# Kernel tuning notes

Hardware: AMD Instinct MI355X
Metric: run time of the kernel (lower is better)

The kernel has to match this reference:

```python
import jax, jax.numpy as jnp
import numpy as np

B, T, M, P, N2 = 16, 8192, 128, 128, 128  # N2 = N//2 complex modes

def setup_inputs() -> dict:
    key = jax.random.key(0)
    k1, k2, k3, k4, k5 = jax.random.split(key, 5)
    u = jax.random.normal(k1, (B, T, M), dtype=jnp.float32)
    # log-parametrized Lambda (S5 'log' convention): Lambda = -exp(row0) + 1j*row1
    log_re = jnp.log(jax.random.uniform(k2, (N2,), minval=0.1, maxval=1.0))
    im = jnp.pi * jnp.arange(N2, dtype=jnp.float32)  # HiPPO-like imaginary spread
    Lambda_param = jnp.stack([log_re, im], axis=0).astype(jnp.float32)
    B_param = jax.random.normal(k3, (2, N2, M), dtype=jnp.float32) / np.sqrt(M)
    C_param = jax.random.normal(k4, (2, P, N2), dtype=jnp.float32) / np.sqrt(N2)
    delta = jnp.array([0.01], dtype=jnp.float32)  # default_\u0394
    return {"u": u, "Lambda_param": Lambda_param, "B_param": B_param,
            "C_param": C_param, "delta": delta}

def reference(u, Lambda_param, B_param, C_param, delta):
    # Reconstruct complex continuous-time matrices
    Lam = (-jnp.exp(Lambda_param[0]) + 1j * Lambda_param[1]).astype(jnp.complex64)   # (N2,)
    Bc = (B_param[0] + 1j * B_param[1]).astype(jnp.complex64)                        # (N2, M)
    Cc = (C_param[0] + 1j * C_param[1]).astype(jnp.complex64)                        # (P, N2)
    d = delta[0]
    # ZOH discretization: Lambda_d = exp(Lam*d), Bd = ((Lambda_d - 1)/Lam) * B
    Ld = jnp.exp(Lam * d)                                                            # (N2,)
    Bd = ((Ld - 1.0) / Lam)[:, None] * Bc                                            # (N2, M)
    # Input projection: Bu[b,t,n] = sum_m u[b,t,m] * Bd[n,m]
    Bu = jnp.einsum('btm,nm->btn', u.astype(jnp.complex64), Bd)                      # (B,T,N2)
    # Parallel scan of x_{k+1} = Ld * x_k + Bu_k, x_0 = 0 -> x holds x_1..x_T
    A = jnp.broadcast_to(Ld, Bu.shape)
    def comb(e1, e2):
        a1, b1 = e1
        a2, b2 = e2
        return (a1 * a2, a2 * b1 + b2)
    _, x = jax.lax.associative_scan(comb, (A, Bu), axis=1)                           # (B,T,N2)
    # return_next_y=True: y_k = 2*Re(C x_{k+1})
    y = 2.0 * jnp.real(jnp.einsum('btn,pn->btp', x, Cc))                             # (B,T,P)
    return y
```

## Files before the change

kernel.cpp:

```cpp
#include <hip/hip_runtime.h>
#include <hip/hip_bf16.h>

#define LCH 128
#define NCH 64
#define NCHUNKS 1024

typedef __attribute__((ext_vector_type(8))) short short8v;
typedef __attribute__((ext_vector_type(4))) short short4v;
typedef __attribute__((ext_vector_type(4))) float f32x4;

#define W2_LDINV 0
#define W2_LDP   16384
#define W2_E     32768
#define W2_CIN   163840
#define WS_WPACK_BYTE  (589824 * 4)
#define WS_CCPACK_BYTE (589824 * 4 + 65536)

#define BUS_BYTE(s, np) ((((s) >> 3) * 4096) + ((np) * 16) + (((s) & 7) * 2))

__device__ inline unsigned short f2bf(float f) {
    union { __hip_bfloat16 h; unsigned short u; } v;
    v.h = __float2bfloat16(f);
    return v.u;
}
__device__ inline short4v pack4(float a, float b, float c, float d) {
    union { __hip_bfloat162 h2[2]; short4v s4; } pk;
    pk.h2[0] = __float22bfloat162_rn(make_float2(a, b));
    pk.h2[1] = __float22bfloat162_rn(make_float2(c, d));
    return pk.s4;
}

__global__ void k0_pows(const float* __restrict__ lp, const float* __restrict__ delta,
                        float2* __restrict__ ws2) {
    const int r = blockIdx.x;
    const int tid = threadIdx.x;
    const int n = tid & 127;
    const double d = (double)delta[0];
    const double lre = -exp((double)lp[n]);
    const double lim = (double)lp[128 + n];
    const double kk = (double)(r + 1) * d;
    if (tid < 128) {
        const double mag = exp(-lre * kk);
        ws2[W2_LDINV + r * 128 + n] = make_float2((float)(mag * cos(lim * kk)),
                                                  (float)(-mag * sin(lim * kk)));
    } else {
        const double mag = exp(lre * kk);
        ws2[W2_LDP + r * 128 + n] = make_float2((float)(mag * cos(lim * kk)),
                                                (float)(mag * sin(lim * kk)));
    }
}

__global__ void k0_wpack(const float* __restrict__ lp, const float* __restrict__ bp,
                         const float* __restrict__ delta, unsigned short* __restrict__ wpack) {
    const int gid = blockIdx.x * 512 + threadIdx.x;
    const int j = gid & 7;
    const int lane = (gid >> 3) & 63;
    const int ks = (gid >> 9) & 3;
    const int ntile = gid >> 11;
    const int np = ntile * 16 + (lane & 15);
    const int m = ks * 32 + ((lane >> 4) & 3) * 8 + j;
    const int n = np & 127;
    const double d = (double)delta[0];
    const double lre = -exp((double)lp[n]);
    const double lim = (double)lp[128 + n];
    const double er = exp(lre * d);
    const double ldr = er * cos(lim * d), ldi = er * sin(lim * d);
    const double nr = ldr - 1.0, ni = ldi;
    const double den = lre * lre + lim * lim;
    const double cr = (nr * lre + ni * lim) / den;
    const double ci = (ni * lre - nr * lim) / den;
    const double br = (double)bp[n * 128 + m];
    const double bi = (double)bp[16384 + n * 128 + m];
    const double v = (np < 128) ? (cr * br - ci * bi) : (cr * bi + ci * br);
    wpack[gid] = f2bf((float)v);
}

__global__ void k0_cpack(const float* __restrict__ cp, unsigned short* __restrict__ ccpack) {
    const int gid = blockIdx.x * 512 + threadIdx.x;
    const int j = gid & 7;
    const int lane = (gid >> 3) & 63;
    const int ks = (gid >> 9) & 7;
    const int ptile = gid >> 12;
    const int p = ptile * 16 + (lane & 15);
    const int k = ks * 32 + ((lane >> 4) & 3) * 8 + j;
    const int n = k >> 1;
    const float v = ((k & 1) == 0) ? 2.0f * cp[p * 128 + n] : -2.0f * cp[16384 + p * 128 + n];
    ccpack[gid] = f2bf(v);
}

__device__ inline void stage_u(const float* __restrict__ uchunk, unsigned short* lds_u) {
    const float4* uf = (const float4*)uchunk;
    const int tid = threadIdx.x;
#pragma unroll
    for (int it = 0; it < 8; ++it) {
        const int f4 = it * 512 + tid;
        const float4 v = uf[f4];
        const int t = f4 >> 5;
        const int m = (f4 & 31) * 4;
        const int byte = (t * 256 + m * 2) ^ ((t & 7) << 4);
        *(short4v*)((char*)lds_u + byte) = pack4(v.x, v.y, v.z, v.w);
    }
}

__global__ __launch_bounds__(512, 4) void k1_end(const float* __restrict__ u,
                                                 float2* __restrict__ ws2,
                                                 const unsigned short* __restrict__ wpack) {
    __shared__ unsigned short lds_u[16384];
    const int tid = threadIdx.x;
    const int lane = tid & 63;
    const int w = tid >> 6;
    const int tl = lane & 15;
    const int gq = (lane >> 4) & 3;
    const int g = blockIdx.x;
    const int b = g >> 6;
    const int c = g & 63;
    const int n = w * 16 + tl;
    stage_u(u + (size_t)(b * 8192 + c * 128) * 128, lds_u);
    __syncthreads();
    const short8v* wp = (const short8v*)wpack;
    float er = 0.f, ei = 0.f;
#pragma unroll
    for (int h = 0; h < 2; ++h) {
        f32x4 acc[4][2];
#pragma unroll
        for (int i = 0; i < 4; ++i) { acc[i][0] = (f32x4)0.f; acc[i][1] = (f32x4)0.f; }
        __builtin_amdgcn_s_setprio(1);
#pragma unroll
        for (int ks = 0; ks < 4; ++ks) {
            const short8v b0 = wp[(w * 4 + ks) * 64 + lane];
            const short8v b1 = wp[((8 + w) * 4 + ks) * 64 + lane];
#pragma unroll
            for (int tt2 = 0; tt2 < 4; ++tt2) {
                const int t = (h * 4 + tt2) * 16 + tl;
                const int byte = (t * 256 + (ks * 32 + gq * 8) * 2) ^ ((t & 7) << 4);
                const short8v a = *(const short8v*)((const char*)lds_u + byte);
                acc[tt2][0] = __builtin_amdgcn_mfma_f32_16x16x32_bf16(a, b0, acc[tt2][0], 0, 0, 0);
                acc[tt2][1] = __builtin_amdgcn_mfma_f32_16x16x32_bf16(a, b1, acc[tt2][1], 0, 0, 0);
            }
        }
        __builtin_amdgcn_s_setprio(0);
        __builtin_amdgcn_sched_barrier(0);
#pragma unroll
        for (int tt2 = 0; tt2 < 4; ++tt2) {
#pragma unroll
            for (int reg = 0; reg < 4; ++reg) {
                const int r = (h * 4 + tt2) * 16 + gq * 4 + reg;
                const float2 li = ws2[W2_LDINV + r * 128 + n];
                const float br = acc[tt2][0][reg], bi = acc[tt2][1][reg];
                er += li.x * br - li.y * bi;
                ei += li.x * bi + li.y * br;
            }
        }
        __builtin_amdgcn_sched_barrier(0);
    }
    er += __shfl_xor(er, 16); ei += __shfl_xor(ei, 16);
    er += __shfl_xor(er, 32); ei += __shfl_xor(ei, 32);
    const float2 ld = ws2[W2_LDP + 127 * 128 + n];
    if (lane < 16) {
        ws2[W2_E + g * 128 + n] = make_float2(ld.x * er - ld.y * ei,
                                              ld.x * ei + ld.y * er);
    }
}

__global__ void k2_carry(float2* __restrict__ ws2) {
    const int idx = blockIdx.x * 256 + threadIdx.x;
    const int b = idx >> 7;
    const int n = idx & 127;
    const float2 l = ws2[W2_LDP + 127 * 128 + n];
    float cr = 0.f, ci = 0.f;
    for (int c = 0; c < NCH; ++c) {
        const int o = (b * NCH + c) * 128 + n;
        ws2[W2_CIN + o] = make_float2(cr, ci);
        const float2 e = ws2[W2_E + o];
        const float nr = fmaf(l.x, cr, fmaf(-l.y, ci, e.x));
        const float ni = fmaf(l.x, ci, fmaf(l.y, cr, e.y));
        cr = nr; ci = ni;
    }
}

__global__ __launch_bounds__(512, 4) void k3_main(const float* __restrict__ u,
                                                  const float2* __restrict__ ws2,
                                                  const unsigned short* __restrict__ wpack,
                                                  const unsigned short* __restrict__ ccpack,
                                                  float* __restrict__ y) {
    __shared__ unsigned short lds[32768];
    unsigned short* lds_u = lds;
    const int tid = threadIdx.x;
    const int lane = tid & 63;
    const int w = tid >> 6;
    const int tl = lane & 15;
    const int gq = (lane >> 4) & 3;
    const int g = blockIdx.x;
    const int b = g >> 6;
    const int c = g & 63;
    const int n = w * 16 + tl;

    stage_u(u + (size_t)(b * 8192 + c * 128) * 128, lds_u);
    __syncthreads();

    const short8v* wp = (const short8v*)wpack;
#pragma unroll
    for (int hh = 0; hh < 2; ++hh) {
        const int h = 1 - hh;
        f32x4 acc[4][2];
#pragma unroll
        for (int i = 0; i < 4; ++i) { acc[i][0] = (f32x4)0.f; acc[i][1] = (f32x4)0.f; }
        __builtin_amdgcn_s_setprio(1);
#pragma unroll
        for (int ks = 0; ks < 4; ++ks) {
            const short8v b0 = wp[(w * 4 + ks) * 64 + lane];
            const short8v b1 = wp[((8 + w) * 4 + ks) * 64 + lane];
#pragma unroll
            for (int tt2 = 0; tt2 < 4; ++tt2) {
                const int t = (h * 4 + tt2) * 16 + tl;
                const int byte = (t * 256 + (ks * 32 + gq * 8) * 2) ^ ((t & 7) << 4);
                const short8v a = *(const short8v*)((const char*)lds_u + byte);
                acc[tt2][0] = __builtin_amdgcn_mfma_f32_16x16x32_bf16(a, b0, acc[tt2][0], 0, 0, 0);
                acc[tt2][1] = __builtin_amdgcn_mfma_f32_16x16x32_bf16(a, b1, acc[tt2][1], 0, 0, 0);
            }
        }
        __builtin_amdgcn_s_setprio(0);
        __builtin_amdgcn_sched_barrier(0);
        if (h == 0) __syncthreads();
#pragma unroll
        for (int tt2 = 0; tt2 < 4; ++tt2) {
            float vr[4], vi[4];
#pragma unroll
            for (int reg = 0; reg < 4; ++reg) {
                const int r = (h * 4 + tt2) * 16 + gq * 4 + reg;
                const float2 li = ws2[W2_LDINV + r * 128 + n];
                const float br = acc[tt2][0][reg], bi = acc[tt2][1][reg];
                vr[reg] = li.x * br - li.y * bi;
                vi[reg] = li.x * bi + li.y * br;
            }
            const int s0 = (h * 4 + tt2) * 16 + gq * 4;
            const int rowr = w * 16 + tl;
            const int rowi = 128 + rowr;
            *(short4v*)((char*)lds + BUS_BYTE(s0, rowr)) = pack4(vr[0], vr[1], vr[2], vr[3]);
            *(short4v*)((char*)lds + BUS_BYTE(s0, rowi)) = pack4(vi[0], vi[1], vi[2], vi[3]);
        }
        __builtin_amdgcn_sched_barrier(0);
    }

    short8v ONES, D0, D1;
#pragma unroll
    for (int j = 0; j < 8; ++j) {
        const int sl = gq * 8 + j;
        ONES[j] = (short)0x3F80;
        D0[j] = (sl <= tl) ? (short)0x3F80 : (short)0;
        D1[j] = (sl <= tl + 16) ? (short)0x3F80 : (short)0;
    }
    f32x4 z[8][2];
#pragma unroll
    for (int i = 0; i < 8; ++i) { z[i][0] = (f32x4)0.f; z[i][1] = (f32x4)0.f; }
#pragma unroll
    for (int ks = 0; ks < 4; ++ks) {
        const int sb = ks * 32 + gq * 8;
        const int rowr = w * 16 + tl;
        const int rowi = 128 + rowr;
        const short8v b0 = *(const short8v*)((const char*)lds + BUS_BYTE(sb, rowr));
        const short8v b1 = *(const short8v*)((const char*)lds + BUS_BYTE(sb, rowi));
#pragma unroll
        for (int tt = 0; tt < 8; ++tt) {
            if (tt < 2 * ks) continue;
            const short8v a = (tt == 2 * ks) ? D0 : ((tt == 2 * ks + 1) ? D1 : ONES);
            z[tt][0] = __builtin_amdgcn_mfma_f32_16x16x32_bf16(a, b0, z[tt][0], 0, 0, 0);
            z[tt][1] = __builtin_amdgcn_mfma_f32_16x16x32_bf16(a, b1, z[tt][1], 0, 0, 0);
        }
    }
    __syncthreads();

    const float2 cin = ws2[W2_CIN + g * 128 + n];
#pragma unroll
    for (int tt = 0; tt < 8; ++tt) {
#pragma unroll
        for (int reg = 0; reg < 4; ++reg) {
            const int r = tt * 16 + gq * 4 + reg;
            const float2 ld = ws2[W2_LDP + r * 128 + n];
            const float zr = z[tt][0][reg] + cin.x;
            const float zi = z[tt][1][reg] + cin.y;
            const float xr = ld.x * zr - ld.y * zi;
            const float xi = ld.x * zi + ld.y * zr;
            union { __hip_bfloat162 h2; unsigned uu; } pk;
            pk.h2 = __float22bfloat162_rn(make_float2(xr, xi));
            const int byte = (r * 512 + n * 4) ^ ((r & 7) << 4);
            *(unsigned*)((char*)lds + byte) = pk.uu;
        }
    }
    __syncthreads();

    const short8v* cc = (const short8v*)ccpack;
    f32x4 yac[8];
#pragma unroll
    for (int i = 0; i < 8; ++i) yac[i] = (f32x4)0.f;
    __builtin_amdgcn_s_setprio(1);
#pragma unroll
    for (int ks = 0; ks < 8; ++ks) {
        const short8v bfrg = cc[(w * 8 + ks) * 64 + lane];
#pragma unroll
        for (int tt = 0; tt < 8; ++tt) {
            const int t = tt * 16 + tl;
            const int byte = (t * 512 + (ks * 32 + gq * 8) * 2) ^ ((t & 7) << 4);
            const short8v a = *(const short8v*)((const char*)lds + byte);
            yac[tt] = __builtin_amdgcn_mfma_f32_16x16x32_bf16(a, bfrg, yac[tt], 0, 0, 0);
        }
    }
    __builtin_amdgcn_s_setprio(0);
    const int p = w * 16 + tl;
    float* yrow = y + (size_t)(b * 8192 + c * 128) * 128;
#pragma unroll
    for (int tt = 0; tt < 8; ++tt) {
#pragma unroll
        for (int reg = 0; reg < 4; ++reg) {
            const int t = tt * 16 + gq * 4 + reg;
            yrow[t * 128 + p] = yac[tt][reg];
        }
    }
}

extern "C" void kernel_launch(void* const* d_in, const int* in_sizes, int n_in,
                              void* d_out, int out_size, void* d_ws, size_t ws_size,
                              hipStream_t stream) {
    const float* u     = (const float*)d_in[0];
    const float* lp    = (const float*)d_in[1];
    const float* bp    = (const float*)d_in[2];
    const float* cp    = (const float*)d_in[3];
    const float* delta = (const float*)d_in[4];
    float* y  = (float*)d_out;
    float2* ws2 = (float2*)d_ws;
    unsigned short* wpack  = (unsigned short*)((char*)d_ws + WS_WPACK_BYTE);
    unsigned short* ccpack = (unsigned short*)((char*)d_ws + WS_CCPACK_BYTE);

    k0_pows <<<128, 256, 0, stream>>>(lp, delta, ws2);
    k0_wpack<<<64, 512, 0, stream>>>(lp, bp, delta, wpack);
    k0_cpack<<<64, 512, 0, stream>>>(cp, ccpack);
    k1_end  <<<NCHUNKS, 512, 0, stream>>>(u, ws2, wpack);
    k2_carry<<<8, 256, 0, stream>>>(ws2);
    k3_main <<<NCHUNKS, 512, 0, stream>>>(u, ws2, wpack, ccpack, y);
}
```

Measured before the change: 88.36 us.

## Process two chunks per block and prefetch next chunk's input into registers

k1_end and k3_main now handle CPB=2 consecutive chunks per workgroup, so half as many blocks are launched. The next chunk's u tile is loaded into registers while the current chunk is being computed, hiding global load latency behind the MFMA work. The cost is extra register pressure from holding the prefetched float4 values and more barriers per block. With 512 blocks on a GPU with many CUs, occupancy and parallelism drop.

```diff
diff --git a/kernel.cpp b/kernel.cpp
--- a/kernel.cpp
+++ b/kernel.cpp
@@ -4,6 +4,7 @@
 #define LCH 128
 #define NCH 64
 #define NCHUNKS 1024
+#define CPB 2
 
 typedef __attribute__((ext_vector_type(8))) short short8v;
 typedef __attribute__((ext_vector_type(4))) short short4v;
@@ -88,17 +89,15 @@
     ccpack[gid] = f2bf(v);
 }
 
-__device__ inline void stage_u(const float* __restrict__ uchunk, unsigned short* lds_u) {
-    const float4* uf = (const float4*)uchunk;
+__device__ inline void stage_regs(const float4* pre, unsigned short* lds_u) {
     const int tid = threadIdx.x;
 #pragma unroll
     for (int it = 0; it < 8; ++it) {
         const int f4 = it * 512 + tid;
-        const float4 v = uf[f4];
         const int t = f4 >> 5;
         const int m = (f4 & 31) * 4;
         const int byte = (t * 256 + m * 2) ^ ((t & 7) << 4);
-        *(short4v*)((char*)lds_u + byte) = pack4(v.x, v.y, v.z, v.w);
+        *(short4v*)((char*)lds_u + byte) = pack4(pre[it].x, pre[it].y, pre[it].z, pre[it].w);
     }
 }
 
@@ -111,54 +110,73 @@
     const int w = tid >> 6;
     const int tl = lane & 15;
     const int gq = (lane >> 4) & 3;
-    const int g = blockIdx.x;
-    const int b = g >> 6;
-    const int c = g & 63;
+    const int g0 = blockIdx.x * CPB;
+    const int b = g0 >> 6;
+    const int c0 = g0 & 63;
     const int n = w * 16 + tl;
-    stage_u(u + (size_t)(b * 8192 + c * 128) * 128, lds_u);
-    __syncthreads();
     const short8v* wp = (const short8v*)wpack;
-    float er = 0.f, ei = 0.f;
-#pragma unroll
-    for (int h = 0; h < 2; ++h) {
-        f32x4 acc[4][2];
-#pragma unroll
-        for (int i = 0; i < 4; ++i) { acc[i][0] = (f32x4)0.f; acc[i][1] = (f32x4)0.f; }
-        __builtin_amdgcn_s_setprio(1);
-#pragma unroll
-        for (int ks = 0; ks < 4; ++ks) {
-            const short8v b0 = wp[(w * 4 + ks) * 64 + lane];
-            const short8v b1 = wp[((8 + w) * 4 + ks) * 64 + lane];
+
+    float4 pre[8];
+    {
+        const float4* uf = (const float4*)(u + (size_t)(b * 8192 + c0 * 128) * 128);
+#pragma unroll
+        for (int it = 0; it < 8; ++it) pre[it] = uf[it * 512 + tid];
+    }
+
+#pragma unroll
+    for (int cc = 0; cc < CPB; ++cc) {
+        const int g = g0 + cc;
+        __syncthreads();
+        stage_regs(pre, lds_u);
+        __syncthreads();
+        if (cc + 1 < CPB) {
+            const float4* uf1 = (const float4*)(u + (size_t)(b * 8192 + (c0 + cc + 1) * 128) * 128);
+#pragma unroll
+            for (int it = 0; it < 8; ++it) pre[it] = uf1[it * 512 + tid];
+            __builtin_amdgcn_sched_barrier(0);
+        }
+        float er = 0.f, ei = 0.f;
+#pragma unroll
+        for (int h = 0; h < 2; ++h) {
+            f32x4 acc[4][2];
+#pragma unroll
+            for (int i = 0; i < 4; ++i) { acc[i][0] = (f32x4)0.f; acc[i][1] = (f32x4)0.f; }
+            __builtin_amdgcn_s_setprio(1);
+#pragma unroll
+            for (int ks = 0; ks < 4; ++ks) {
+                const short8v b0 = wp[(w * 4 + ks) * 64 + lane];
+                const short8v b1 = wp[((8 + w) * 4 + ks) * 64 + lane];
+#pragma unroll
+                for (int tt2 = 0; tt2 < 4; ++tt2) {
+                    const int t = (h * 4 + tt2) * 16 + tl;
+                    const int byte = (t * 256 + (ks * 32 + gq * 8) * 2) ^ ((t & 7) << 4);
+                    const short8v a = *(const short8v*)((const char*)lds_u + byte);
+                    acc[tt2][0] = __builtin_amdgcn_mfma_f32_16x16x32_bf16(a, b0, acc[tt2][0], 0, 0, 0);
+                    acc[tt2][1] = __builtin_amdgcn_mfma_f32_16x16x32_bf16(a, b1, acc[tt2][1], 0, 0, 0);
+                }
+            }
+            __builtin_amdgcn_s_setprio(0);
+            __builtin_amdgcn_sched_barrier(0);
 #pragma unroll
             for (int tt2 = 0; tt2 < 4; ++tt2) {
-                const int t = (h * 4 + tt2) * 16 + tl;
-                const int byte = (t * 256 + (ks * 32 + gq * 8) * 2) ^ ((t & 7) << 4);
-                const short8v a = *(const short8v*)((const char*)lds_u + byte);
-                acc[tt2][0] = __builtin_amdgcn_mfma_f32_16x16x32_bf16(a, b0, acc[tt2][0], 0, 0, 0);
-                acc[tt2][1] = __builtin_amdgcn_mfma_f32_16x16x32_bf16(a, b1, acc[tt2][1], 0, 0, 0);
-            }
-        }
-        __builtin_amdgcn_s_setprio(0);
-        __builtin_amdgcn_sched_barrier(0);
-#pragma unroll
-        for (int tt2 = 0; tt2 < 4; ++tt2) {
-#pragma unroll
-            for (int reg = 0; reg < 4; ++reg) {
-                const int r = (h * 4 + tt2) * 16 + gq * 4 + reg;
-                const float2 li = ws2[W2_LDINV + r * 128 + n];
-                const float br = acc[tt2][0][reg], bi = acc[tt2][1][reg];
-                er += li.x * br - li.y * bi;
-                ei += li.x * bi + li.y * br;
-            }
-        }
-        __builtin_amdgcn_sched_barrier(0);
-    }
-    er += __shfl_xor(er, 16); ei += __shfl_xor(ei, 16);
-    er += __shfl_xor(er, 32); ei += __shfl_xor(ei, 32);
-    const float2 ld = ws2[W2_LDP + 127 * 128 + n];
-    if (lane < 16) {
-        ws2[W2_E + g * 128 + n] = make_float2(ld.x * er - ld.y * ei,
-                                              ld.x * ei + ld.y * er);
+#pragma unroll
+                for (int reg = 0; reg < 4; ++reg) {
+                    const int r = (h * 4 + tt2) * 16 + gq * 4 + reg;
+                    const float2 li = ws2[W2_LDINV + r * 128 + n];
+                    const float br = acc[tt2][0][reg], bi = acc[tt2][1][reg];
+                    er += li.x * br - li.y * bi;
+                    ei += li.x * bi + li.y * br;
+                }
+            }
+            __builtin_amdgcn_sched_barrier(0);
+        }
+        er += __shfl_xor(er, 16); ei += __shfl_xor(ei, 16);
+        er += __shfl_xor(er, 32); ei += __shfl_xor(ei, 32);
+        const float2 ld = ws2[W2_LDP + 127 * 128 + n];
+        if (lane < 16) {
+            ws2[W2_E + g * 128 + n] = make_float2(ld.x * er - ld.y * ei,
+                                                  ld.x * ei + ld.y * er);
+        }
     }
 }
 
@@ -184,136 +202,155 @@
                                                   const unsigned short* __restrict__ ccpack,
                                                   float* __restrict__ y) {
     __shared__ unsigned short lds[32768];
-    unsigned short* lds_u = lds;
     const int tid = threadIdx.x;
     const int lane = tid & 63;
     const int w = tid >> 6;
     const int tl = lane & 15;
     const int gq = (lane >> 4) & 3;
-    const int g = blockIdx.x;
-    const int b = g >> 6;
-    const int c = g & 63;
+    const int g0 = blockIdx.x * CPB;
+    const int b = g0 >> 6;
+    const int c0 = g0 & 63;
     const int n = w * 16 + tl;
-
-    stage_u(u + (size_t)(b * 8192 + c * 128) * 128, lds_u);
-    __syncthreads();
-
     const short8v* wp = (const short8v*)wpack;
-#pragma unroll
-    for (int hh = 0; hh < 2; ++hh) {
-        const int h = 1 - hh;
-        f32x4 acc[4][2];
-#pragma unroll
-        for (int i = 0; i < 4; ++i) { acc[i][0] = (f32x4)0.f; acc[i][1] = (f32x4)0.f; }
-        __builtin_amdgcn_s_setprio(1);
+    const short8v* cc8 = (const short8v*)ccpack;
+
+    float4 pre[8];
+    {
+        const float4* uf = (const float4*)(u + (size_t)(b * 8192 + c0 * 128) * 128);
+#pragma unroll
+        for (int it = 0; it < 8; ++it) pre[it] = uf[it * 512 + tid];
+    }
+
+#pragma unroll
+    for (int cc = 0; cc < CPB; ++cc) {
+        const int g = g0 + cc;
+        const int c = c0 + cc;
+        __syncthreads();
+        stage_regs(pre, lds);
+        __syncthreads();
+
+#pragma unroll
+        for (int hh = 0; hh < 2; ++hh) {
+            const int h = 1 - hh;
+            f32x4 acc[4][2];
+#pragma unroll
+            for (int i = 0; i < 4; ++i) { acc[i][0] = (f32x4)0.f; acc[i][1] = (f32x4)0.f; }
+            __builtin_amdgcn_s_setprio(1);
+#pragma unroll
+            for (int ks = 0; ks < 4; ++ks) {
+                const short8v b0 = wp[(w * 4 + ks) * 64 + lane];
+                const short8v b1 = wp[((8 + w) * 4 + ks) * 64 + lane];
+#pragma unroll
+                for (int tt2 = 0; tt2 < 4; ++tt2) {
+                    const int t = (h * 4 + tt2) * 16 + tl;
+                    const int byte = (t * 256 + (ks * 32 + gq * 8) * 2) ^ ((t & 7) << 4);
+                    const short8v a = *(const short8v*)((const char*)lds + byte);
+                    acc[tt2][0] = __builtin_amdgcn_mfma_f32_16x16x32_bf16(a, b0, acc[tt2][0], 0, 0, 0);
+                    acc[tt2][1] = __builtin_amdgcn_mfma_f32_16x16x32_bf16(a, b1, acc[tt2][1], 0, 0, 0);
+                }
+            }
+            __builtin_amdgcn_s_setprio(0);
+            __builtin_amdgcn_sched_barrier(0);
+            if (h == 0) __syncthreads();
+#pragma unroll
+            for (int tt2 = 0; tt2 < 4; ++tt2) {
+                float vr[4], vi[4];
+#pragma unroll
+                for (int reg = 0; reg < 4; ++reg) {
+                    const int r = (h * 4 + tt2) * 16 + gq * 4 + reg;
+                    const float2 li = ws2[W2_LDINV + r * 128 + n];
+                    const float br = acc[tt2][0][reg], bi = acc[tt2][1][reg];
+                    vr[reg] = li.x * br - li.y * bi;
+                    vi[reg] = li.x * bi + li.y * br;
+                }
+                const int s0 = (h * 4 + tt2) * 16 + gq * 4;
+                const int rowr = w * 16 + tl;
+                const int rowi = 128 + rowr;
+                *(short4v*)((char*)lds + BUS_BYTE(s0, rowr)) = pack4(vr[0], vr[1], vr[2], vr[3]);
+                *(short4v*)((char*)lds + BUS_BYTE(s0, rowi)) = pack4(vi[0], vi[1], vi[2], vi[3]);
+            }
+            __builtin_amdgcn_sched_barrier(0);
+        }
+
+        if (cc + 1 < CPB) {
+            const float4* uf1 = (const float4*)(u + (size_t)(b * 8192 + (c + 1) * 128) * 128);
+#pragma unroll
+            for (int it = 0; it < 8; ++it) pre[it] = uf1[it * 512 + tid];
+            __builtin_amdgcn_sched_barrier(0);
+        }
+
+        short8v ONES, D0, D1;
+#pragma unroll
+        for (int j = 0; j < 8; ++j) {
+            const int sl = gq * 8 + j;
+            ONES[j] = (short)0x3F80;
+            D0[j] = (sl <= tl) ? (short)0x3F80 : (short)0;
+            D1[j] = (sl <= tl + 16) ? (short)0x3F80 : (short)0;
+        }
+        f32x4 z[8][2];
+#pragma unroll
+        for (int i = 0; i < 8; ++i) { z[i][0] = (f32x4)0.f; z[i][1] = (f32x4)0.f; }
 #pragma unroll
         for (int ks = 0; ks < 4; ++ks) {
-            const short8v b0 = wp[(w * 4 + ks) * 64 + lane];
-            const short8v b1 = wp[((8 + w) * 4 + ks) * 64 + lane];
-#pragma unroll
-            for (int tt2 = 0; tt2 < 4; ++tt2) {
-                const int t = (h * 4 + tt2) * 16 + tl;
-                const int byte = (t * 256 + (ks * 32 + gq * 8) * 2) ^ ((t & 7) << 4);
-                const short8v a = *(const short8v*)((const char*)lds_u + byte);
-                acc[tt2][0] = __builtin_amdgcn_mfma_f32_16x16x32_bf16(a, b0, acc[tt2][0], 0, 0, 0);
-                acc[tt2][1] = __builtin_amdgcn_mfma_f32_16x16x32_bf16(a, b1, acc[tt2][1], 0, 0, 0);
-            }
-        }
-        __builtin_amdgcn_s_setprio(0);
-        __builtin_amdgcn_sched_barrier(0);
-        if (h == 0) __syncthreads();
-#pragma unroll
-        for (int tt2 = 0; tt2 < 4; ++tt2) {
-            float vr[4], vi[4];
-#pragma unroll
-            for (int reg = 0; reg < 4; ++reg) {
-                const int r = (h * 4 + tt2) * 16 + gq * 4 + reg;
-                const float2 li = ws2[W2_LDINV + r * 128 + n];
-                const float br = acc[tt2][0][reg], bi = acc[tt2][1][reg];
-                vr[reg] = li.x * br - li.y * bi;
-                vi[reg] = li.x * bi + li.y * br;
-            }
-            const int s0 = (h * 4 + tt2) * 16 + gq * 4;
+            const int sb = ks * 32 + gq * 8;
             const int rowr = w * 16 + tl;
             const int rowi = 128 + rowr;
-            *(short4v*)((char*)lds + BUS_BYTE(s0, rowr)) = pack4(vr[0], vr[1], vr[2], vr[3]);
-            *(short4v*)((char*)lds + BUS_BYTE(s0, rowi)) = pack4(vi[0], vi[1], vi[2], vi[3]);
-        }
-        __builtin_amdgcn_sched_barrier(0);
-    }
-
-    short8v ONES, D0, D1;
-#pragma unroll
-    for (int j = 0; j < 8; ++j) {
-        const int sl = gq * 8 + j;
-        ONES[j] = (short)0x3F80;
-        D0[j] = (sl <= tl) ? (short)0x3F80 : (short)0;
-        D1[j] = (sl <= tl + 16) ? (short)0x3F80 : (short)0;
-    }
-    f32x4 z[8][2];
-#pragma unroll
-    for (int i = 0; i < 8; ++i) { z[i][0] = (f32x4)0.f; z[i][1] = (f32x4)0.f; }
-#pragma unroll
-    for (int ks = 0; ks < 4; ++ks) {
-        const int sb = ks * 32 + gq * 8;
-        const int rowr = w * 16 + tl;
-        const int rowi = 128 + rowr;
-        const short8v b0 = *(const short8v*)((const char*)lds + BUS_BYTE(sb, rowr));
-        const short8v b1 = *(const short8v*)((const char*)lds + BUS_BYTE(sb, rowi));
+            const short8v b0 = *(const short8v*)((const char*)lds + BUS_BYTE(sb, rowr));
+            const short8v b1 = *(const short8v*)((const char*)lds + BUS_BYTE(sb, rowi));
+#pragma unroll
+            for (int tt = 0; tt < 8; ++tt) {
+                if (tt < 2 * ks) continue;
+                const short8v a = (tt == 2 * ks) ? D0 : ((tt == 2 * ks + 1) ? D1 : ONES);
+                z[tt][0] = __builtin_amdgcn_mfma_f32_16x16x32_bf16(a, b0, z[tt][0], 0, 0, 0);
+                z[tt][1] = __builtin_amdgcn_mfma_f32_16x16x32_bf16(a, b1, z[tt][1], 0, 0, 0);
+            }
+        }
+        __syncthreads();
+
+        const float2 cin = ws2[W2_CIN + g * 128 + n];
 #pragma unroll
         for (int tt = 0; tt < 8; ++tt) {
-            if (tt < 2 * ks) continue;
-            const short8v a = (tt == 2 * ks) ? D0 : ((tt == 2 * ks + 1) ? D1 : ONES);
-            z[tt][0] = __builtin_amdgcn_mfma_f32_16x16x32_bf16(a, b0, z[tt][0], 0, 0, 0);
-            z[tt][1] = __builtin_amdgcn_mfma_f32_16x16x32_bf16(a, b1, z[tt][1], 0, 0, 0);
-        }
-    }
-    __syncthreads();
-
-    const float2 cin = ws2[W2_CIN + g * 128 + n];
-#pragma unroll
-    for (int tt = 0; tt < 8; ++tt) {
-#pragma unroll
-        for (int reg = 0; reg < 4; ++reg) {
-            const int r = tt * 16 + gq * 4 + reg;
-            const float2 ld = ws2[W2_LDP + r * 128 + n];
-            const float zr = z[tt][0][reg] + cin.x;
-            const float zi = z[tt][1][reg] + cin.y;
-            const float xr = ld.x * zr - ld.y * zi;
-            const float xi = ld.x * zi + ld.y * zr;
-            union { __hip_bfloat162 h2; unsigned uu; } pk;
-            pk.h2 = __float22bfloat162_rn(make_float2(xr, xi));
-            const int byte = (r * 512 + n * 4) ^ ((r & 7) << 4);
-            *(unsigned*)((char*)lds + byte) = pk.uu;
-        }
-    }
-    __syncthreads();
-
-    const short8v* cc = (const short8v*)ccpack;
-    f32x4 yac[8];
-#pragma unroll
-    for (int i = 0; i < 8; ++i) yac[i] = (f32x4)0.f;
-    __builtin_amdgcn_s_setprio(1);
-#pragma unroll
-    for (int ks = 0; ks < 8; ++ks) {
-        const short8v bfrg = cc[(w * 8 + ks) * 64 + lane];
+#pragma unroll
+            for (int reg = 0; reg < 4; ++reg) {
+                const int r = tt * 16 + gq * 4 + reg;
+                const float2 ld = ws2[W2_LDP + r * 128 + n];
+                const float zr = z[tt][0][reg] + cin.x;
+                const float zi = z[tt][1][reg] + cin.y;
+                const float xr = ld.x * zr - ld.y * zi;
+                const float xi = ld.x * zi + ld.y * zr;
+                union { __hip_bfloat162 h2; unsigned uu; } pk;
+                pk.h2 = __float22bfloat162_rn(make_float2(xr, xi));
+                const int byte = (r * 512 + n * 4) ^ ((r & 7) << 4);
+                *(unsigned*)((char*)lds + byte) = pk.uu;
+            }
+        }
+        __syncthreads();
+
+        f32x4 yac[8];
+#pragma unroll
+        for (int i = 0; i < 8; ++i) yac[i] = (f32x4)0.f;
+        __builtin_amdgcn_s_setprio(1);
+#pragma unroll
+        for (int ks = 0; ks < 8; ++ks) {
+            const short8v bfrg = cc8[(w * 8 + ks) * 64 + lane];
+#pragma unroll
+            for (int tt = 0; tt < 8; ++tt) {
+                const int t = tt * 16 + tl;
+                const int byte = (t * 512 + (ks * 32 + gq * 8) * 2) ^ ((t & 7) << 4);
+                const short8v a = *(const short8v*)((const char*)lds + byte);
+                yac[tt] = __builtin_amdgcn_mfma_f32_16x16x32_bf16(a, bfrg, yac[tt], 0, 0, 0);
+            }
+        }
+        __builtin_amdgcn_s_setprio(0);
+        const int p = w * 16 + tl;
+        float* yrow = y + (size_t)(b * 8192 + c * 128) * 128;
 #pragma unroll
         for (int tt = 0; tt < 8; ++tt) {
-            const int t = tt * 16 + tl;
-            const int byte = (t * 512 + (ks * 32 + gq * 8) * 2) ^ ((t & 7) << 4);
-            const short8v a = *(const short8v*)((const char*)lds + byte);
-            yac[tt] = __builtin_amdgcn_mfma_f32_16x16x32_bf16(a, bfrg, yac[tt], 0, 0, 0);
-        }
-    }
-    __builtin_amdgcn_s_setprio(0);
-    const int p = w * 16 + tl;
-    float* yrow = y + (size_t)(b * 8192 + c * 128) * 128;
-#pragma unroll
-    for (int tt = 0; tt < 8; ++tt) {
-#pragma unroll
-        for (int reg = 0; reg < 4; ++reg) {
-            const int t = tt * 16 + gq * 4 + reg;
-            yrow[t * 128 + p] = yac[tt][reg];
+#pragma unroll
+            for (int reg = 0; reg < 4; ++reg) {
+                const int t = tt * 16 + gq * 4 + reg;
+                yrow[t * 128 + p] = yac[tt][reg];
+            }
         }
     }
 }
@@ -334,7 +371,7 @@
     k0_pows <<<128, 256, 0, stream>>>(lp, delta, ws2);
     k0_wpack<<<64, 512, 0, stream>>>(lp, bp, delta, wpack);
     k0_cpack<<<64, 512, 0, stream>>>(cp, ccpack);
-    k1_end  <<<NCHUNKS, 512, 0, stream>>>(u, ws2, wpack);
+    k1_end  <<<NCHUNKS / CPB, 512, 0, stream>>>(u, ws2, wpack);
     k2_carry<<<8, 256, 0, stream>>>(ws2);
-    k3_main <<<NCHUNKS, 512, 0, stream>>>(u, ws2, wpack, ccpack, y);
-}
+    k3_main <<<NCHUNKS / CPB, 512, 0, stream>>>(u, ws2, wpack, ccpack, y);
+}
```

Measured after the change: 320.2 us. +262.4%, slower.

## Halve scan chunk length to 64, fuse setup kernels, reuse carry buffer in place

Applied to the files above, without the earlier changes.

Chunk length drops from 128 to 64 timesteps, so the grid grows to 2048 blocks with half the LDS each, and launch bounds rise to 6 blocks per CU for more occupancy. The intra-chunk triangular scan does less work per chunk, but the sequential carry pass now walks 128 chunks per batch instead of 64. The three setup kernels are merged into one launch to cut launch overhead, and the carry kernel writes carries over the chunk-end buffer in place instead of using a separate array.

```diff
diff --git a/kernel.cpp b/kernel.cpp
--- a/kernel.cpp
+++ b/kernel.cpp
@@ -1,20 +1,19 @@
 #include <hip/hip_runtime.h>
 #include <hip/hip_bf16.h>
 
-#define LCH 128
-#define NCH 64
-#define NCHUNKS 1024
+#define LCH 64
+#define NCH 128
+#define NCHUNKS 2048
 
 typedef __attribute__((ext_vector_type(8))) short short8v;
 typedef __attribute__((ext_vector_type(4))) short short4v;
 typedef __attribute__((ext_vector_type(4))) float f32x4;
 
 #define W2_LDINV 0
-#define W2_LDP   16384
-#define W2_E     32768
-#define W2_CIN   163840
-#define WS_WPACK_BYTE  (589824 * 4)
-#define WS_CCPACK_BYTE (589824 * 4 + 65536)
+#define W2_LDP   8192
+#define W2_E     16384
+#define WS_WPACK_BYTE  2359296
+#define WS_CCPACK_BYTE (2359296 + 65536)
 
 #define BUS_BYTE(s, np) ((((s) >> 3) * 4096) + ((np) * 16) + (((s) & 7) * 2))
 
@@ -30,132 +29,129 @@
     return pk.s4;
 }
 
-__global__ void k0_pows(const float* __restrict__ lp, const float* __restrict__ delta,
-                        float2* __restrict__ ws2) {
+__global__ void k0_all(const float* __restrict__ lp, const float* __restrict__ bp,
+                       const float* __restrict__ cp, const float* __restrict__ delta,
+                       float2* __restrict__ ws2, unsigned short* __restrict__ wpack,
+                       unsigned short* __restrict__ ccpack) {
     const int r = blockIdx.x;
     const int tid = threadIdx.x;
-    const int n = tid & 127;
-    const double d = (double)delta[0];
-    const double lre = -exp((double)lp[n]);
-    const double lim = (double)lp[128 + n];
-    const double kk = (double)(r + 1) * d;
-    if (tid < 128) {
-        const double mag = exp(-lre * kk);
-        ws2[W2_LDINV + r * 128 + n] = make_float2((float)(mag * cos(lim * kk)),
-                                                  (float)(-mag * sin(lim * kk)));
+    if (r < 64) {
+        if (tid < 256) {
+            const int n = tid & 127;
+            const double d = (double)delta[0];
+            const double lre = -exp((double)lp[n]);
+            const double lim = (double)lp[128 + n];
+            const double kk = (double)(r + 1) * d;
+            if (tid < 128) {
+                const double mag = exp(-lre * kk);
+                ws2[W2_LDINV + r * 128 + n] = make_float2((float)(mag * cos(lim * kk)),
+                                                          (float)(-mag * sin(lim * kk)));
+            } else {
+                const double mag = exp(lre * kk);
+                ws2[W2_LDP + r * 128 + n] = make_float2((float)(mag * cos(lim * kk)),
+                                                        (float)(mag * sin(lim * kk)));
+            }
+        }
+    } else if (r < 128) {
+        const int gid = (r - 64) * 512 + tid;
+        const int j = gid & 7;
+        const int lane = (gid >> 3) & 63;
+        const int ks = (gid >> 9) & 3;
+        const int ntile = gid >> 11;
+        const int np = ntile * 16 + (lane & 15);
+        const int m = ks * 32 + ((lane >> 4) & 3) * 8 + j;
+        const int n = np & 127;
+        const double d = (double)delta[0];
+        const double lre = -exp((double)lp[n]);
+        const double lim = (double)lp[128 + n];
+        const double er = exp(lre * d);
+        const double ldr = er * cos(lim * d), ldi = er * sin(lim * d);
+        const double nr = ldr - 1.0, ni = ldi;
+        const double den = lre * lre + lim * lim;
+        const double cr = (nr * lre + ni * lim) / den;
+        const double ci = (ni * lre - nr * lim) / den;
+        const double br = (double)bp[n * 128 + m];
+        const double bi = (double)bp[16384 + n * 128 + m];
+        const double v = (np < 128) ? (cr * br - ci * bi) : (cr * bi + ci * br);
+        wpack[gid] = f2bf((float)v);
     } else {
-        const double mag = exp(lre * kk);
-        ws2[W2_LDP + r * 128 + n] = make_float2((float)(mag * cos(lim * kk)),
-                                                (float)(mag * sin(lim * kk)));
-    }
-}
-
-__global__ void k0_wpack(const float* __restrict__ lp, const float* __restrict__ bp,
-                         const float* __restrict__ delta, unsigned short* __restrict__ wpack) {
-    const int gid = blockIdx.x * 512 + threadIdx.x;
-    const int j = gid & 7;
-    const int lane = (gid >> 3) & 63;
-    const int ks = (gid >> 9) & 3;
-    const int ntile = gid >> 11;
-    const int np = ntile * 16 + (lane & 15);
-    const int m = ks * 32 + ((lane >> 4) & 3) * 8 + j;
-    const int n = np & 127;
-    const double d = (double)delta[0];
-    const double lre = -exp((double)lp[n]);
-    const double lim = (double)lp[128 + n];
-    const double er = exp(lre * d);
-    const double ldr = er * cos(lim * d), ldi = er * sin(lim * d);
-    const double nr = ldr - 1.0, ni = ldi;
-    const double den = lre * lre + lim * lim;
-    const double cr = (nr * lre + ni * lim) / den;
-    const double ci = (ni * lre - nr * lim) / den;
-    const double br = (double)bp[n * 128 + m];
-    const double bi = (double)bp[16384 + n * 128 + m];
-    const double v = (np < 128) ? (cr * br - ci * bi) : (cr * bi + ci * br);
-    wpack[gid] = f2bf((float)v);
-}
-
-__global__ void k0_cpack(const float* __restrict__ cp, unsigned short* __restrict__ ccpack) {
-    const int gid = blockIdx.x * 512 + threadIdx.x;
-    const int j = gid & 7;
-    const int lane = (gid >> 3) & 63;
-    const int ks = (gid >> 9) & 7;
-    const int ptile = gid >> 12;
-    const int p = ptile * 16 + (lane & 15);
-    const int k = ks * 32 + ((lane >> 4) & 3) * 8 + j;
-    const int n = k >> 1;
-    const float v = ((k & 1) == 0) ? 2.0f * cp[p * 128 + n] : -2.0f * cp[16384 + p * 128 + n];
-    ccpack[gid] = f2bf(v);
-}
-
-__device__ inline void stage_u(const float* __restrict__ uchunk, unsigned short* lds_u) {
-    const float4* uf = (const float4*)uchunk;
-    const int tid = threadIdx.x;
-#pragma unroll
-    for (int it = 0; it < 8; ++it) {
-        const int f4 = it * 512 + tid;
-        const float4 v = uf[f4];
-        const int t = f4 >> 5;
-        const int m = (f4 & 31) * 4;
-        const int byte = (t * 256 + m * 2) ^ ((t & 7) << 4);
-        *(short4v*)((char*)lds_u + byte) = pack4(v.x, v.y, v.z, v.w);
-    }
-}
-
-__global__ __launch_bounds__(512, 4) void k1_end(const float* __restrict__ u,
+        const int gid = (r - 128) * 512 + tid;
+        const int j = gid & 7;
+        const int lane = (gid >> 3) & 63;
+        const int ks = (gid >> 9) & 7;
+        const int ptile = gid >> 12;
+        const int p = ptile * 16 + (lane & 15);
+        const int k = ks * 32 + ((lane >> 4) & 3) * 8 + j;
+        const int n = k >> 1;
+        const float v = ((k & 1) == 0) ? 2.0f * cp[p * 128 + n]
+                                       : -2.0f * cp[16384 + p * 128 + n];
+        ccpack[gid] = f2bf(v);
+    }
+}
+
+__global__ __launch_bounds__(512, 6) void k1_end(const float* __restrict__ u,
                                                  float2* __restrict__ ws2,
                                                  const unsigned short* __restrict__ wpack) {
-    __shared__ unsigned short lds_u[16384];
+    __shared__ unsigned short lds_u[8192];
     const int tid = threadIdx.x;
     const int lane = tid & 63;
     const int w = tid >> 6;
     const int tl = lane & 15;
     const int gq = (lane >> 4) & 3;
     const int g = blockIdx.x;
-    const int b = g >> 6;
-    const int c = g & 63;
+    const int b = g >> 7;
+    const int c = g & 127;
     const int n = w * 16 + tl;
-    stage_u(u + (size_t)(b * 8192 + c * 128) * 128, lds_u);
-    __syncthreads();
     const short8v* wp = (const short8v*)wpack;
+
+    {
+        const float4* uf = (const float4*)(u + (size_t)(b * 8192 + c * LCH) * 128);
+#pragma unroll
+        for (int it = 0; it < 4; ++it) {
+            const int f4 = it * 512 + tid;
+            const float4 v = uf[f4];
+            const int t = f4 >> 5;
+            const int m = (f4 & 31) * 4;
+            const int byte = (t * 256 + m * 2) ^ ((t & 7) << 4);
+            *(short4v*)((char*)lds_u + byte) = pack4(v.x, v.y, v.z, v.w);
+        }
+    }
+    __syncthreads();
+
+    f32x4 acc[4][2];
+#pragma unroll
+    for (int i = 0; i < 4; ++i) { acc[i][0] = (f32x4)0.f; acc[i][1] = (f32x4)0.f; }
+    __builtin_amdgcn_s_setprio(1);
+#pragma unroll
+    for (int ks = 0; ks < 4; ++ks) {
+        const short8v b0 = wp[(w * 4 + ks) * 64 + lane];
+        const short8v b1 = wp[((8 + w) * 4 + ks) * 64 + lane];
+#pragma unroll
+        for (int tt = 0; tt < 4; ++tt) {
+            const int t = tt * 16 + tl;
+            const int byte = (t * 256 + (ks * 32 + gq * 8) * 2) ^ ((t & 7) << 4);
+            const short8v a = *(const short8v*)((const char*)lds_u + byte);
+            acc[tt][0] = __builtin_amdgcn_mfma_f32_16x16x32_bf16(a, b0, acc[tt][0], 0, 0, 0);
+            acc[tt][1] = __builtin_amdgcn_mfma_f32_16x16x32_bf16(a, b1, acc[tt][1], 0, 0, 0);
+        }
+    }
+    __builtin_amdgcn_s_setprio(0);
+
     float er = 0.f, ei = 0.f;
 #pragma unroll
-    for (int h = 0; h < 2; ++h) {
-        f32x4 acc[4][2];
-#pragma unroll
-        for (int i = 0; i < 4; ++i) { acc[i][0] = (f32x4)0.f; acc[i][1] = (f32x4)0.f; }
-        __builtin_amdgcn_s_setprio(1);
-#pragma unroll
-        for (int ks = 0; ks < 4; ++ks) {
-            const short8v b0 = wp[(w * 4 + ks) * 64 + lane];
-            const short8v b1 = wp[((8 + w) * 4 + ks) * 64 + lane];
-#pragma unroll
-            for (int tt2 = 0; tt2 < 4; ++tt2) {
-                const int t = (h * 4 + tt2) * 16 + tl;
-                const int byte = (t * 256 + (ks * 32 + gq * 8) * 2) ^ ((t & 7) << 4);
-                const short8v a = *(const short8v*)((const char*)lds_u + byte);
-                acc[tt2][0] = __builtin_amdgcn_mfma_f32_16x16x32_bf16(a, b0, acc[tt2][0], 0, 0, 0);
-                acc[tt2][1] = __builtin_amdgcn_mfma_f32_16x16x32_bf16(a, b1, acc[tt2][1], 0, 0, 0);
-            }
-        }
-        __builtin_amdgcn_s_setprio(0);
-        __builtin_amdgcn_sched_barrier(0);
-#pragma unroll
-        for (int tt2 = 0; tt2 < 4; ++tt2) {
-#pragma unroll
-            for (int reg = 0; reg < 4; ++reg) {
-                const int r = (h * 4 + tt2) * 16 + gq * 4 + reg;
-                const float2 li = ws2[W2_LDINV + r * 128 + n];
-                const float br = acc[tt2][0][reg], bi = acc[tt2][1][reg];
-                er += li.x * br - li.y * bi;
-                ei += li.x * bi + li.y * br;
-            }
-        }
-        __builtin_amdgcn_sched_barrier(0);
+    for (int tt = 0; tt < 4; ++tt) {
+#pragma unroll
+        for (int reg = 0; reg < 4; ++reg) {
+            const int r = tt * 16 + gq * 4 + reg;
+            const float2 li = ws2[W2_LDINV + r * 128 + n];
+            const float br = acc[tt][0][reg], bi = acc[tt][1][reg];
+            er += li.x * br - li.y * bi;
+            ei += li.x * bi + li.y * br;
+        }
     }
     er += __shfl_xor(er, 16); ei += __shfl_xor(ei, 16);
     er += __shfl_xor(er, 32); ei += __shfl_xor(ei, 32);
-    const float2 ld = ws2[W2_LDP + 127 * 128 + n];
+    const float2 ld = ws2[W2_LDP + 63 * 128 + n];
     if (lane < 16) {
         ws2[W2_E + g * 128 + n] = make_float2(ld.x * er - ld.y * ei,
                                               ld.x * ei + ld.y * er);
@@ -166,81 +162,106 @@
     const int idx = blockIdx.x * 256 + threadIdx.x;
     const int b = idx >> 7;
     const int n = idx & 127;
-    const float2 l = ws2[W2_LDP + 127 * 128 + n];
+    const float2 l = ws2[W2_LDP + 63 * 128 + n];
     float cr = 0.f, ci = 0.f;
     for (int c = 0; c < NCH; ++c) {
         const int o = (b * NCH + c) * 128 + n;
-        ws2[W2_CIN + o] = make_float2(cr, ci);
         const float2 e = ws2[W2_E + o];
+        ws2[W2_E + o] = make_float2(cr, ci);
         const float nr = fmaf(l.x, cr, fmaf(-l.y, ci, e.x));
         const float ni = fmaf(l.x, ci, fmaf(l.y, cr, e.y));
         cr = nr; ci = ni;
     }
 }
 
-__global__ __launch_bounds__(512, 4) void k3_main(const float* __restrict__ u,
+__global__ __launch_bounds__(512, 6) void k3_main(const float* __restrict__ u,
                                                   const float2* __restrict__ ws2,
                                                   const unsigned short* __restrict__ wpack,
                                                   const unsigned short* __restrict__ ccpack,
                                                   float* __restrict__ y) {
-    __shared__ unsigned short lds[32768];
-    unsigned short* lds_u = lds;
+    __shared__ unsigned short lds[16384];
     const int tid = threadIdx.x;
     const int lane = tid & 63;
     const int w = tid >> 6;
     const int tl = lane & 15;
     const int gq = (lane >> 4) & 3;
     const int g = blockIdx.x;
-    const int b = g >> 6;
-    const int c = g & 63;
+    const int b = g >> 7;
+    const int c = g & 127;
     const int n = w * 16 + tl;
-
-    stage_u(u + (size_t)(b * 8192 + c * 128) * 128, lds_u);
-    __syncthreads();
-
     const short8v* wp = (const short8v*)wpack;
-#pragma unroll
-    for (int hh = 0; hh < 2; ++hh) {
-        const int h = 1 - hh;
-        f32x4 acc[4][2];
-#pragma unroll
-        for (int i = 0; i < 4; ++i) { acc[i][0] = (f32x4)0.f; acc[i][1] = (f32x4)0.f; }
-        __builtin_amdgcn_s_setprio(1);
-#pragma unroll
-        for (int ks = 0; ks < 4; ++ks) {
-            const short8v b0 = wp[(w * 4 + ks) * 64 + lane];
-            const short8v b1 = wp[((8 + w) * 4 + ks) * 64 + lane];
-#pragma unroll
-            for (int tt2 = 0; tt2 < 4; ++tt2) {
-                const int t = (h * 4 + tt2) * 16 + tl;
-                const int byte = (t * 256 + (ks * 32 + gq * 8) * 2) ^ ((t & 7) << 4);
-                const short8v a = *(const short8v*)((const char*)lds_u + byte);
-                acc[tt2][0] = __builtin_amdgcn_mfma_f32_16x16x32_bf16(a, b0, acc[tt2][0], 0, 0, 0);
-                acc[tt2][1] = __builtin_amdgcn_mfma_f32_16x16x32_bf16(a, b1, acc[tt2][1], 0, 0, 0);
-            }
-        }
-        __builtin_amdgcn_s_setprio(0);
-        __builtin_amdgcn_sched_barrier(0);
-        if (h == 0) __syncthreads();
-#pragma unroll
-        for (int tt2 = 0; tt2 < 4; ++tt2) {
-            float vr[4], vi[4];
-#pragma unroll
-            for (int reg = 0; reg < 4; ++reg) {
-                const int r = (h * 4 + tt2) * 16 + gq * 4 + reg;
-                const float2 li = ws2[W2_LDINV + r * 128 + n];
-                const float br = acc[tt2][0][reg], bi = acc[tt2][1][reg];
-                vr[reg] = li.x * br - li.y * bi;
-                vi[reg] = li.x * bi + li.y * br;
-            }
-            const int s0 = (h * 4 + tt2) * 16 + gq * 4;
-            const int rowr = w * 16 + tl;
-            const int rowi = 128 + rowr;
-            *(short4v*)((char*)lds + BUS_BYTE(s0, rowr)) = pack4(vr[0], vr[1], vr[2], vr[3]);
-            *(short4v*)((char*)lds + BUS_BYTE(s0, rowi)) = pack4(vi[0], vi[1], vi[2], vi[3]);
-        }
-        __builtin_amdgcn_sched_barrier(0);
-    }
+    const short8v* cc8 = (const short8v*)ccpack;
+
+    {
+        const float4* uf = (const float4*)(u + (size_t)(b * 8192 + c * LCH) * 128);
+#pragma unroll
+        for (int it = 0; it < 4; ++it) {
+            const int f4 = it * 512 + tid;
+            const float4 v = uf[f4];
+            const int t = f4 >> 5;
+            const int m = (f4 & 31) * 4;
+            const int byte = (t * 256 + m * 2) ^ ((t & 7) << 4);
+            *(short4v*)((char*)lds + byte) = pack4(v.x, v.y, v.z, v.w);
+        }
+    }
+    __syncthreads();
+
+    f32x4 acc[4][2];
+#pragma unroll
+    for (int i = 0; i < 4; ++i) { acc[i][0] = (f32x4)0.f; acc[i][1] = (f32x4)0.f; }
+    __builtin_amdgcn_s_setprio(1);
+#pragma unroll
+    for (int ks = 0; ks < 4; ++ks) {
+        const short8v b0 = wp[(w * 4 + ks) * 64 + lane];
+        const short8v b1 = wp[((8 + w) * 4 + ks) * 64 + lane];
+#pragma unroll
+        for (int tt = 0; tt < 4; ++tt) {
+            const int t = tt * 16 + tl;
+            const int byte = (t * 256 + (ks * 32 + gq * 8) * 2) ^ ((t & 7) << 4);
+            const short8v a = *(const short8v*)((const char*)lds + byte);
+            acc[tt][0] = __builtin_amdgcn_mfma_f32_16x16x32_bf16(a, b0, acc[tt][0], 0, 0, 0);
+            acc[tt][1] = __builtin_amdgcn_mfma_f32_16x16x32_bf16(a, b1, acc[tt][1], 0, 0, 0);
+        }
+    }
+    __builtin_amdgcn_s_setprio(0);
+    __builtin_amdgcn_sched_barrier(0);
+
+#pragma unroll
+    for (int tt = 2; tt < 4; ++tt) {
+        float vr[4], vi[4];
+#pragma unroll
+        for (int reg = 0; reg < 4; ++reg) {
+            const int r = tt * 16 + gq * 4 + reg;
+            const float2 li = ws2[W2_LDINV + r * 128 + n];
+            const float br = acc[tt][0][reg], bi = acc[tt][1][reg];
+            vr[reg] = li.x * br - li.y * bi;
+            vi[reg] = li.x * bi + li.y * br;
+        }
+        const int s0 = tt * 16 + gq * 4;
+        const int rowr = w * 16 + tl;
+        const int rowi = 128 + rowr;
+        *(short4v*)((char*)lds + BUS_BYTE(s0, rowr)) = pack4(vr[0], vr[1], vr[2], vr[3]);
+        *(short4v*)((char*)lds + BUS_BYTE(s0, rowi)) = pack4(vi[0], vi[1], vi[2], vi[3]);
+    }
+    __syncthreads();
+#pragma unroll
+    for (int tt = 0; tt < 2; ++tt) {
+        float vr[4], vi[4];
+#pragma unroll
+        for (int reg = 0; reg < 4; ++reg) {
+            const int r = tt * 16 + gq * 4 + reg;
+            const float2 li = ws2[W2_LDINV + r * 128 + n];
+            const float br = acc[tt][0][reg], bi = acc[tt][1][reg];
+            vr[reg] = li.x * br - li.y * bi;
+            vi[reg] = li.x * bi + li.y * br;
+        }
+        const int s0 = tt * 16 + gq * 4;
+        const int rowr = w * 16 + tl;
+        const int rowi = 128 + rowr;
+        *(short4v*)((char*)lds + BUS_BYTE(s0, rowr)) = pack4(vr[0], vr[1], vr[2], vr[3]);
+        *(short4v*)((char*)lds + BUS_BYTE(s0, rowi)) = pack4(vi[0], vi[1], vi[2], vi[3]);
+    }
+    __builtin_amdgcn_sched_barrier(0);
 
     short8v ONES, D0, D1;
 #pragma unroll
@@ -250,18 +271,18 @@
         D0[j] = (sl <= tl) ? (short)0x3F80 : (short)0;
         D1[j] = (sl <= tl + 16) ? (short)0x3F80 : (short)0;
     }
-    f32x4 z[8][2];
-#pragma unroll
-    for (int i = 0; i < 8; ++i) { z[i][0] = (f32x4)0.f; z[i][1] = (f32x4)0.f; }
-#pragma unroll
-    for (int ks = 0; ks < 4; ++ks) {
+    f32x4 z[4][2];
+#pragma unroll
+    for (int i = 0; i < 4; ++i) { z[i][0] = (f32x4)0.f; z[i][1] = (f32x4)0.f; }
+#pragma unroll
+    for (int ks = 0; ks < 2; ++ks) {
         const int sb = ks * 32 + gq * 8;
         const int rowr = w * 16 + tl;
         const int rowi = 128 + rowr;
         const short8v b0 = *(const short8v*)((const char*)lds + BUS_BYTE(sb, rowr));
         const short8v b1 = *(const short8v*)((const char*)lds + BUS_BYTE(sb, rowi));
 #pragma unroll
-        for (int tt = 0; tt < 8; ++tt) {
+        for (int tt = 0; tt < 4; ++tt) {
             if (tt < 2 * ks) continue;
             const short8v a = (tt == 2 * ks) ? D0 : ((tt == 2 * ks + 1) ? D1 : ONES);
             z[tt][0] = __builtin_amdgcn_mfma_f32_16x16x32_bf16(a, b0, z[tt][0], 0, 0, 0);
@@ -270,9 +291,9 @@
     }
     __syncthreads();
 
-    const float2 cin = ws2[W2_CIN + g * 128 + n];
-#pragma unroll
-    for (int tt = 0; tt < 8; ++tt) {
+    const float2 cin = ws2[W2_E + g * 128 + n];
+#pragma unroll
+    for (int tt = 0; tt < 4; ++tt) {
 #pragma unroll
         for (int reg = 0; reg < 4; ++reg) {
             const int r = tt * 16 + gq * 4 + reg;
@@ -289,16 +310,15 @@
     }
     __syncthreads();
 
-    const short8v* cc = (const short8v*)ccpack;
-    f32x4 yac[8];
-#pragma unroll
-    for (int i = 0; i < 8; ++i) yac[i] = (f32x4)0.f;
+    f32x4 yac[4];
+#pragma unroll
+    for (int i = 0; i < 4; ++i) yac[i] = (f32x4)0.f;
     __builtin_amdgcn_s_setprio(1);
 #pragma unroll
     for (int ks = 0; ks < 8; ++ks) {
-        const short8v bfrg = cc[(w * 8 + ks) * 64 + lane];
-#pragma unroll
-        for (int tt = 0; tt < 8; ++tt) {
+        const short8v bfrg = cc8[(w * 8 + ks) * 64 + lane];
+#pragma unroll
+        for (int tt = 0; tt < 4; ++tt) {
             const int t = tt * 16 + tl;
             const int byte = (t * 512 + (ks * 32 + gq * 8) * 2) ^ ((t & 7) << 4);
             const short8v a = *(const short8v*)((const char*)lds + byte);
@@ -307,9 +327,9 @@
     }
     __builtin_amdgcn_s_setprio(0);
     const int p = w * 16 + tl;
-    float* yrow = y + (size_t)(b * 8192 + c * 128) * 128;
-#pragma unroll
-    for (int tt = 0; tt < 8; ++tt) {
+    float* yrow = y + (size_t)(b * 8192 + c * LCH) * 128;
+#pragma unroll
+    for (int tt = 0; tt < 4; ++tt) {
 #pragma unroll
         for (int reg = 0; reg < 4; ++reg) {
             const int t = tt * 16 + gq * 4 + reg;
@@ -331,9 +351,7 @@
     unsigned short* wpack  = (unsigned short*)((char*)d_ws + WS_WPACK_BYTE);
     unsigned short* ccpack = (unsigned short*)((char*)d_ws + WS_CCPACK_BYTE);
 
-    k0_pows <<<128, 256, 0, stream>>>(lp, delta, ws2);
-    k0_wpack<<<64, 512, 0, stream>>>(lp, bp, delta, wpack);
-    k0_cpack<<<64, 512, 0, stream>>>(cp, ccpack);
+    k0_all  <<<192, 512, 0, stream>>>(lp, bp, cp, delta, ws2, wpack, ccpack);
     k1_end  <<<NCHUNKS, 512, 0, stream>>>(u, ws2, wpack);
     k2_carry<<<8, 256, 0, stream>>>(ws2);
     k3_main <<<NCHUNKS, 512, 0, stream>>>(u, ws2, wpack, ccpack, y);
```

After: 97.85 us. 10.7% more time.
